# Kernel optimization log

Hardware: AMD Instinct MI355X
Metric: run time of the kernel (lower is better)

The kernel has to match this reference:

```python
import jax, jax.numpy as jnp
import numpy as np

S = 72
IMG_W, IMG_H = 640, 360
STRIDE = 32
FMAP_H, FMAP_W = IMG_H // STRIDE, IMG_W // STRIDE  # 11, 20
N_OFFSETS = S
N_STRIPS = S - 1
ANGLES = np.array([15.0, 22.0, 30.0, 39.0, 49.0, 60.0, 72.0, 80.0, 90.0, 100.0, 108.0, 120.0, 131.0, 141.0, 150.0, 158.0, 165.0])
N_ANG = 17
N_PRED = 2 + 2 + 1 + N_OFFSETS  # 77
N_EDGE = FMAP_W + 2 * FMAP_H    # 42
N_PROP = N_ANG * N_EDGE         # 714
NMS_THRES = 15.0
BACKBONE_C = 512
CONV_C = 1024


def _make_anchors():
    anchor_ys = np.linspace(1.0, 0.0, N_OFFSETS)
    tan = np.tan(np.deg2rad(ANGLES))
    def side(origins):
        out = np.zeros((N_ANG, N_PRED, len(origins)), np.float32)
        for i, (sx, sy) in enumerate(origins):
            out[:, 2, i] = 1.0 - sy
            out[:, 3, i] = sx
            out[:, 5:, i] = (sx + (sy - anchor_ys)[None, :] / tan[:, None]) * IMG_W
        return out.reshape(N_ANG * N_PRED, len(origins))
    left = side([(0.0, y) for y in np.linspace(1.0, 0.0, FMAP_H)])
    right = side([(1.0, y) for y in np.linspace(1.0, 0.0, FMAP_H)])
    bottom = side([(x, 1.0) for x in np.linspace(1.0, 0.0, FMAP_W)])
    anchors = np.zeros((N_ANG * N_PRED, FMAP_H, FMAP_W), np.float32)
    anchors[:, :, 0] = left
    anchors[:, :, -1] = right
    anchors[:, -1, :] = bottom
    edge = np.concatenate([anchors[:, :, 0], anchors[:, :, -1], anchors[:, -1, :]], 1)  # [1309,42]
    anch_dim = edge.reshape(N_ANG, N_PRED, N_EDGE).transpose(2, 0, 1).reshape(N_PROP, N_PRED)
    return jnp.asarray(anchors), jnp.asarray(anch_dim)


def setup_inputs():
    key = jax.random.key(0)
    ks = jax.random.split(key, 4)
    B = 32
    feat = jax.random.normal(ks[0], (B, BACKBONE_C, FMAP_H, FMAP_W), jnp.float32)
    W_conv = jax.random.normal(ks[1], (CONV_C, BACKBONE_C), jnp.float32) * 0.02
    b_conv = jnp.zeros((CONV_C,), jnp.float32)
    W_cls = jax.random.normal(ks[2], (2 * N_ANG, CONV_C), jnp.float32) * 0.02
    b_cls = jnp.zeros((2 * N_ANG,), jnp.float32)
    W_reg = jax.random.normal(ks[3], (N_ANG * (N_OFFSETS + 1), CONV_C), jnp.float32) * 0.02
    b_reg = jnp.zeros((N_ANG * (N_OFFSETS + 1),), jnp.float32)
    anchors, anchors_anchor_dim = _make_anchors()
    return {"feat": feat, "W_conv": W_conv, "b_conv": b_conv, "W_cls": W_cls, "b_cls": b_cls,
            "W_reg": W_reg, "b_reg": b_reg, "anchors": anchors, "anchors_anchor_dim": anchors_anchor_dim}


def _proposals(feat, W_conv, b_conv, W_cls, b_cls, W_reg, b_reg, anchors):
    B = feat.shape[0]
    features = jnp.einsum('bchw,oc->bohw', feat, W_conv) + b_conv[None, :, None, None]
    cls_f = jnp.einsum('bchw,oc->bohw', features, W_cls) + b_cls[None, :, None, None]
    reg_f = jnp.einsum('bchw,oc->bohw', features, W_reg) + b_reg[None, :, None, None]
    anch = anchors.reshape(N_ANG, N_PRED, FMAP_H, FMAP_W)
    cls_r = cls_f.reshape(B, N_ANG, 2, FMAP_H, FMAP_W)
    reg_r = reg_f.reshape(B, N_ANG, N_OFFSETS + 1, FMAP_H, FMAP_W)
    # slots 0:2 <- cls logits (set), slots 2:4 <- anchor (copied), slots 4: <- anchor + reg
    mid = jnp.broadcast_to(anch[None, :, 2:4], (B, N_ANG, 2, FMAP_H, FMAP_W))
    tail = anch[None, :, 4:] + reg_r
    lane = jnp.concatenate([cls_r, mid, tail], axis=2)  # [B,17,77,h,w]
    # gather the three feature-map edges: left col, right col, bottom row
    edges = jnp.concatenate([lane[:, :, :, :, 0], lane[:, :, :, :, -1], lane[:, :, :, -1, :]], axis=3)  # [B,17,77,42]
    return edges.transpose(0, 3, 1, 2).reshape(B, N_PROP, N_PRED)  # [B,714,77]


def _nms_one(props, scores):
    # greedy line-NMS over proposals of one image, shapes static
    order = jnp.argsort(-scores)
    p = props[order]
    start = jnp.clip(jnp.round(p[:, 2] * N_STRIPS), 0.0, float(N_STRIPS))
    end = jnp.clip(start + p[:, 4] - 1.0, 0.0, float(N_STRIPS))
    xs = p[:, 5:]  # [N,72]
    s = jnp.maximum(start[:, None], start[None, :])
    e = jnp.minimum(end[:, None], end[None, :])
    idx = jnp.arange(N_OFFSETS, dtype=p.dtype)
    m = (idx[None, None, :] >= s[..., None]) & (idx[None, None, :] <= e[..., None])  # [N,N,72]
    diff = jnp.abs(xs[:, None, :] - xs[None, :, :])  # [N,N,72]
    cnt = e - s + 1.0
    dist = jnp.where(cnt > 0, jnp.sum(diff * m, -1) / jnp.maximum(cnt, 1.0), jnp.inf)
    sup = dist < NMS_THRES
    n = p.shape[0]
    pos = jnp.arange(n)
    def step(suppressed, i):
        keep_i = ~suppressed[i]
        suppressed = suppressed | (keep_i & sup[i] & (pos > i))
        return suppressed, keep_i
    _, keep_sorted = jax.lax.scan(step, jnp.zeros(n, bool), pos)
    return jnp.zeros(n, bool).at[order].set(keep_sorted)


def reference(feat, W_conv, b_conv, W_cls, b_cls, W_reg, b_reg, anchors, anchors_anchor_dim):
    proposals = _proposals(feat, W_conv, b_conv, W_cls, b_cls, W_reg, b_reg, anchors)
    scores = jax.nn.softmax(proposals[..., :2], axis=-1)[..., 1]  # [B,714]
    keep_mask = jax.lax.map(lambda pr: _nms_one(pr[0], pr[1]), (proposals, scores))  # [B,714]
    return proposals, keep_mask, scores
```

## Files before the change

kernel.cpp:

```cpp
#include <hip/hip_runtime.h>
#include <math.h>

#define NB     32
#define FH     11
#define FW     20
#define CIN    512
#define CMID   1024
#define NANG   17
#define NPREDD 77
#define NEDGE  42
#define NPROPP 714
#define NOFF   72
#define NCLS   34
#define NREGR  1241
#define N2PAD  1280
#define MTOT   1344
#define NSTRIPSF 71.0f
#define PADK   40

typedef unsigned long long u64;
typedef unsigned short ushortt;
typedef short s8v __attribute__((ext_vector_type(8)));
typedef float f4v __attribute__((ext_vector_type(4)));

__device__ inline ushortt f2bf(float f) {
    unsigned u = __float_as_uint(f);
    u += 0x7fffu + ((u >> 16) & 1u);
    return (ushortt)(u >> 16);
}
__device__ inline float bf2f(ushortt h) {
    return __uint_as_float(((unsigned)h) << 16);
}

__global__ __launch_bounds__(256) void k_gather_split(const float* __restrict__ feat,
                                                      ushortt* __restrict__ Ahi,
                                                      ushortt* __restrict__ Alo)
{
    int idx = blockIdx.x * 256 + threadIdx.x;
    int m = idx >> 9, c = idx & 511;
    int b = m / NEDGE, e = m - b * NEDGE;
    int h, w;
    if (e < FH)          { h = e;      w = 0;      }
    else if (e < 2 * FH) { h = e - FH; w = FW - 1; }
    else                 { h = FH - 1; w = e - 2 * FH; }
    float v = feat[((size_t)(b * CIN + c) * FH + h) * FW + w];
    ushortt hi = f2bf(v);
    Ahi[idx] = hi;
    Alo[idx] = f2bf(v - bf2f(hi));
}

__global__ __launch_bounds__(256) void k_gemm1m(const ushortt* __restrict__ Ahi,
                                                const ushortt* __restrict__ Alo,
                                                const float* __restrict__ W,
                                                const float* __restrict__ bias,
                                                ushortt* __restrict__ Chi,
                                                ushortt* __restrict__ Clo)
{
    const int K = CIN, N = CMID;
    __shared__ __align__(16) ushortt Ash[64 * PADK], Asl[64 * PADK];
    __shared__ __align__(16) ushortt Bsh[64 * PADK], Bsl[64 * PADK];
    int tid = threadIdx.x;
    int m0 = blockIdx.y * 64, n0 = blockIdx.x * 64;
    int srow = tid >> 2, sg = tid & 3;
    int lane = tid & 63, wv = tid >> 6;
    int wm = (wv & 1) * 32, wn = (wv >> 1) * 32;
    int quad = lane >> 4, l15 = lane & 15;

    f4v acc[2][2];
#pragma unroll
    for (int i = 0; i < 2; ++i)
#pragma unroll
        for (int j = 0; j < 2; ++j) acc[i][j] = (f4v){0.f, 0.f, 0.f, 0.f};

    const ushortt* Ahp = Ahi + (size_t)(m0 + srow) * K + sg * 8;
    const ushortt* Alp = Alo + (size_t)(m0 + srow) * K + sg * 8;
    const float*   Wp  = W   + (size_t)(n0 + srow) * K + sg * 8;

    for (int k0 = 0; k0 < K; k0 += 32) {
        __syncthreads();
        s8v av = *(const s8v*)(Ahp + k0);
        s8v lv = *(const s8v*)(Alp + k0);
        float4 w0 = *(const float4*)(Wp + k0);
        float4 w1 = *(const float4*)(Wp + k0 + 4);
        float wf[8] = {w0.x, w0.y, w0.z, w0.w, w1.x, w1.y, w1.z, w1.w};
        s8v wh, wl;
#pragma unroll
        for (int j = 0; j < 8; ++j) {
            ushortt h = f2bf(wf[j]);
            wh[j] = (short)h;
            wl[j] = (short)f2bf(wf[j] - bf2f(h));
        }
        *(s8v*)&Ash[srow * PADK + sg * 8] = av;
        *(s8v*)&Asl[srow * PADK + sg * 8] = lv;
        *(s8v*)&Bsh[srow * PADK + sg * 8] = wh;
        *(s8v*)&Bsl[srow * PADK + sg * 8] = wl;
        __syncthreads();
        s8v ah[2], al[2], bh[2], bl[2];
#pragma unroll
        for (int s = 0; s < 2; ++s) {
            ah[s] = *(const s8v*)&Ash[(wm + s * 16 + l15) * PADK + quad * 8];
            al[s] = *(const s8v*)&Asl[(wm + s * 16 + l15) * PADK + quad * 8];
            bh[s] = *(const s8v*)&Bsh[(wn + s * 16 + l15) * PADK + quad * 8];
            bl[s] = *(const s8v*)&Bsl[(wn + s * 16 + l15) * PADK + quad * 8];
        }
#pragma unroll
        for (int sm = 0; sm < 2; ++sm)
#pragma unroll
            for (int sn = 0; sn < 2; ++sn) {
                acc[sm][sn] = __builtin_amdgcn_mfma_f32_16x16x32_bf16(al[sm], bl[sn], acc[sm][sn], 0, 0, 0);
                acc[sm][sn] = __builtin_amdgcn_mfma_f32_16x16x32_bf16(al[sm], bh[sn], acc[sm][sn], 0, 0, 0);
                acc[sm][sn] = __builtin_amdgcn_mfma_f32_16x16x32_bf16(ah[sm], bl[sn], acc[sm][sn], 0, 0, 0);
                acc[sm][sn] = __builtin_amdgcn_mfma_f32_16x16x32_bf16(ah[sm], bh[sn], acc[sm][sn], 0, 0, 0);
            }
    }
#pragma unroll
    for (int sm = 0; sm < 2; ++sm)
#pragma unroll
        for (int sn = 0; sn < 2; ++sn)
#pragma unroll
            for (int r = 0; r < 4; ++r) {
                int m = m0 + wm + sm * 16 + quad * 4 + r;
                int n = n0 + wn + sn * 16 + l15;
                float v = acc[sm][sn][r] + bias[n];
                ushortt h = f2bf(v);
                Chi[(size_t)m * N + n] = h;
                Clo[(size_t)m * N + n] = f2bf(v - bf2f(h));
            }
}

__global__ __launch_bounds__(256) void k_gemm2m(const ushortt* __restrict__ Ahi,
                                                const ushortt* __restrict__ Alo,
                                                const float* __restrict__ Wcls,
                                                const float* __restrict__ bcls,
                                                const float* __restrict__ Wreg,
                                                const float* __restrict__ breg,
                                                float* __restrict__ C)
{
    const int K = CMID;
    __shared__ __align__(16) ushortt Ash[64 * PADK], Asl[64 * PADK];
    __shared__ __align__(16) ushortt Bsh[64 * PADK], Bsl[64 * PADK];
    int tid = threadIdx.x;
    int m0 = blockIdx.y * 64, n0 = blockIdx.x * 64;
    int srow = tid >> 2, sg = tid & 3;
    int lane = tid & 63, wv = tid >> 6;
    int wm = (wv & 1) * 32, wn = (wv >> 1) * 32;
    int quad = lane >> 4, l15 = lane & 15;

    f4v acc[2][2];
#pragma unroll
    for (int i = 0; i < 2; ++i)
#pragma unroll
        for (int j = 0; j < 2; ++j) acc[i][j] = (f4v){0.f, 0.f, 0.f, 0.f};

    const ushortt* Ahp = Ahi + (size_t)(m0 + srow) * K + sg * 8;
    const ushortt* Alp = Alo + (size_t)(m0 + srow) * K + sg * 8;
    int nrow = n0 + srow;
    const float* Wp = Wcls;
    bool wvalid = true;
    if (nrow < NCLS)              Wp = Wcls + (size_t)nrow * K + sg * 8;
    else if (nrow < NCLS + NREGR) Wp = Wreg + (size_t)(nrow - NCLS) * K + sg * 8;
    else                          wvalid = false;

    for (int k0 = 0; k0 < K; k0 += 32) {
        __syncthreads();
        s8v av = *(const s8v*)(Ahp + k0);
        s8v lv = *(const s8v*)(Alp + k0);
        float4 w0, w1;
        if (wvalid) {
            w0 = *(const float4*)(Wp + k0);
            w1 = *(const float4*)(Wp + k0 + 4);
        } else {
            w0 = make_float4(0.f, 0.f, 0.f, 0.f);
            w1 = w0;
        }
        float wf[8] = {w0.x, w0.y, w0.z, w0.w, w1.x, w1.y, w1.z, w1.w};
        s8v wh, wl;
#pragma unroll
        for (int j = 0; j < 8; ++j) {
            ushortt h = f2bf(wf[j]);
            wh[j] = (short)h;
            wl[j] = (short)f2bf(wf[j] - bf2f(h));
        }
        *(s8v*)&Ash[srow * PADK + sg * 8] = av;
        *(s8v*)&Asl[srow * PADK + sg * 8] = lv;
        *(s8v*)&Bsh[srow * PADK + sg * 8] = wh;
        *(s8v*)&Bsl[srow * PADK + sg * 8] = wl;
        __syncthreads();
        s8v ah[2], al[2], bh[2], bl[2];
#pragma unroll
        for (int s = 0; s < 2; ++s) {
            ah[s] = *(const s8v*)&Ash[(wm + s * 16 + l15) * PADK + quad * 8];
            al[s] = *(const s8v*)&Asl[(wm + s * 16 + l15) * PADK + quad * 8];
            bh[s] = *(const s8v*)&Bsh[(wn + s * 16 + l15) * PADK + quad * 8];
            bl[s] = *(const s8v*)&Bsl[(wn + s * 16 + l15) * PADK + quad * 8];
        }
#pragma unroll
        for (int sm = 0; sm < 2; ++sm)
#pragma unroll
            for (int sn = 0; sn < 2; ++sn) {
                acc[sm][sn] = __builtin_amdgcn_mfma_f32_16x16x32_bf16(al[sm], bl[sn], acc[sm][sn], 0, 0, 0);
                acc[sm][sn] = __builtin_amdgcn_mfma_f32_16x16x32_bf16(al[sm], bh[sn], acc[sm][sn], 0, 0, 0);
                acc[sm][sn] = __builtin_amdgcn_mfma_f32_16x16x32_bf16(ah[sm], bl[sn], acc[sm][sn], 0, 0, 0);
                acc[sm][sn] = __builtin_amdgcn_mfma_f32_16x16x32_bf16(ah[sm], bh[sn], acc[sm][sn], 0, 0, 0);
            }
    }
#pragma unroll
    for (int sm = 0; sm < 2; ++sm)
#pragma unroll
        for (int sn = 0; sn < 2; ++sn)
#pragma unroll
            for (int r = 0; r < 4; ++r) {
                int m = m0 + wm + sm * 16 + quad * 4 + r;
                int n = n0 + wn + sn * 16 + l15;
                float bb = (n < NCLS) ? bcls[n] : ((n < NCLS + NREGR) ? breg[n - NCLS] : 0.f);
                C[(size_t)m * N2PAD + n] = acc[sm][sn][r] + bb;
            }
}

__global__ __launch_bounds__(256) void k_assemble(const float* __restrict__ C2,
                                                  const float* __restrict__ AD,
                                                  float* __restrict__ outP,
                                                  float* __restrict__ outS,
                                                  float* __restrict__ startv,
                                                  float* __restrict__ endv,
                                                  float* __restrict__ xsel)
{
    int mb = blockIdx.x;
    int b = mb / NEDGE, e = mb - b * NEDGE;
    const float* c2 = C2 + (size_t)mb * N2PAD;
    int tid = threadIdx.x;
    for (int idx = tid; idx < NANG * NPREDD; idx += 256) {
        int a = idx / NPREDD, p = idx - a * NPREDD;
        int prop = e * NANG + a;
        float v;
        if (p < 2) v = c2[a * 2 + p];
        else {
            v = AD[prop * NPREDD + p];
            if (p >= 4) v += c2[NCLS + a * 73 + (p - 4)];
        }
        outP[((size_t)b * NPROPP + prop) * NPREDD + p] = v;
    }
    if (tid < NANG) {
        int a = tid, prop = e * NANG + a;
        float c0 = c2[2 * a], c1 = c2[2 * a + 1];
        float mx = fmaxf(c0, c1);
        float e0 = expf(c0 - mx), e1 = expf(c1 - mx);
        outS[b * NPROPP + prop] = e1 / (e0 + e1);
        float p2 = AD[prop * NPREDD + 2];
        float p4 = AD[prop * NPREDD + 4] + c2[NCLS + a * 73];
        float st = fminf(fmaxf(rintf(p2 * NSTRIPSF), 0.0f), NSTRIPSF);
        float en = fminf(fmaxf(st + p4 - 1.0f, 0.0f), NSTRIPSF);
        startv[b * 720 + prop] = st;
        endv[b * 720 + prop] = en;
        int ksi = (int)st;
        xsel[b * 720 + prop] = AD[prop * NPREDD + 5 + ksi] + c2[NCLS + a * 73 + ksi + 1];
    }
}

__global__ __launch_bounds__(128) void k_sort(const float* __restrict__ scores,
                                              int* __restrict__ order)
{
    int b = blockIdx.x, tile = blockIdx.y, tid = threadIdx.x;
    __shared__ __align__(16) float s[720];
    for (int x = tid; x < 720; x += 128)
        s[x] = (x < NPROPP) ? scores[b * NPROPP + x] : -1e30f;
    __syncthreads();
    int i = tile * 128 + tid;
    if (i >= NPROPP) return;
    float si = s[i];
    int r = 0;
#pragma unroll 4
    for (int j4 = 0; j4 < 720; j4 += 4) {
        float4 v = *(const float4*)&s[j4];
        r += (v.x > si) || (v.x == si && (j4 + 0) < i);
        r += (v.y > si) || (v.y == si && (j4 + 1) < i);
        r += (v.z > si) || (v.z == si && (j4 + 2) < i);
        r += (v.w > si) || (v.w == si && (j4 + 3) < i);
    }
    order[b * 720 + r] = i;
}

__global__ __launch_bounds__(256) void k_supmat(const float* __restrict__ outP,
                                                const float* __restrict__ startv,
                                                const float* __restrict__ endv,
                                                const float* __restrict__ xsel,
                                                const int* __restrict__ order,
                                                u64* __restrict__ sup)
{
    int jt = blockIdx.x, it = blockIdx.y, b = blockIdx.z;
    int i0 = it * 64, j0 = jt * 64;
    int tid = threadIdx.x;
    if (j0 + 63 < i0) {
        if (tid < 64) {
            int il = i0 + tid;
            if (il < NPROPP) sup[((size_t)b * NPROPP + il) * 12 + jt] = 0ull;
        }
        return;
    }
    __shared__ float SI[64], EI[64], XI[64];
    __shared__ float SJ[64], EJ[64], XJ[64];
    __shared__ int   OI[64], OJ[64];
    if (tid < 128) {
        int side = tid >> 6, q = tid & 63;
        int pos = (side ? j0 : i0) + q;
        int o = (pos < NPROPP) ? order[b * 720 + pos] : -1;
        float st = (o >= 0) ? startv[b * 720 + o] : 0.f;
        float en = (o >= 0) ? endv[b * 720 + o] : -2.f;
        float xv = (o >= 0) ? xsel[b * 720 + o] : 0.f;
        if (!side) { SI[q] = st; EI[q] = en; XI[q] = xv; OI[q] = o; }
        else       { SJ[q] = st; EJ[q] = en; XJ[q] = xv; OJ[q] = o; }
    }
    __syncthreads();
    int lane = tid & 63, w = tid >> 6;
    int j = j0 + lane;
    float sj = SJ[lane], ej = EJ[lane], xj = XJ[lane];
    const float* basexs = outP + (size_t)b * NPROPP * NPREDD + 5;
#pragma unroll 1
    for (int rep = 0; rep < 16; ++rep) {
        int iloc = w * 16 + rep;
        int il = i0 + iloc;
        float si = SI[iloc], ei = EI[iloc];
        float s = fmaxf(si, sj), e = fminf(ei, ej);
        float cnt = e - s + 1.0f;
        bool sp = false;
        if (cnt > 0.f) {
            if (e < s) {
                sp = true;
            } else {
                int ks = (int)s, ke = (int)e;
                if (si == sj && ke == ks) {
                    sp = (fabsf(XI[iloc] - xj) / fmaxf(cnt, 1.0f)) < 15.0f;
                } else {
                    const float* xi  = basexs + (size_t)OI[iloc] * NPREDD;
                    const float* xjp = basexs + (size_t)OJ[lane] * NPREDD;
                    float sum = 0.f;
                    for (int k = ks; k <= ke; ++k)
                        sum += fabsf(xi[k] - xjp[k]);
                    sp = (sum / fmaxf(cnt, 1.0f)) < 15.0f;
                }
            }
        }
        bool valid = (il < NPROPP) && (j < NPROPP) && (j > il);
        u64 msk = __ballot(valid && sp);
        if (lane == 0 && il < NPROPP)
            sup[((size_t)b * NPROPP + il) * 12 + jt] = msk;
    }
}

__global__ __launch_bounds__(256) void k_scan(const u64* __restrict__ sup,
                                              const int* __restrict__ order,
                                              float* __restrict__ keep_out)
{
    int b = blockIdx.x, tid = threadIdx.x;
    int lane = tid & 63;
    __shared__ u64 K[12], NS[12];
    __shared__ int changed;
    const u64* base = sup + (size_t)b * NPROPP * 12;

    int r0 = tid, r1 = tid + 256, r2 = tid + 512;
    u64 row0[12], row1[12], row2[12];
#pragma unroll
    for (int t = 0; t < 12; ++t) {
        row0[t] = base[(size_t)r0 * 12 + t];
        row1[t] = (r1 < NPROPP) ? base[(size_t)r1 * 12 + t] : 0ull;
        row2[t] = (r2 < NPROPP) ? base[(size_t)r2 * 12 + t] : 0ull;
    }
    if (tid < 12) {
        K[tid] = (tid < 11) ? ~0ull : ((1ull << (NPROPP - 704)) - 1ull);
        NS[tid] = 0ull;
    }
    __syncthreads();

    for (int sweep = 0; sweep < 720; ++sweep) {
        u64 m0 = 0ull - ((K[r0 >> 6] >> (r0 & 63)) & 1ull);
        u64 m1 = (r1 < NPROPP) ? (0ull - ((K[r1 >> 6] >> (r1 & 63)) & 1ull)) : 0ull;
        u64 m2 = (r2 < NPROPP) ? (0ull - ((K[r2 >> 6] >> (r2 & 63)) & 1ull)) : 0ull;
        unsigned lo[12], hi[12];
#pragma unroll
        for (int t = 0; t < 12; ++t) {
            u64 a = (row0[t] & m0) | (row1[t] & m1) | (row2[t] & m2);
            lo[t] = (unsigned)a;
            hi[t] = (unsigned)(a >> 32);
        }
#pragma unroll
        for (int s = 1; s < 64; s <<= 1) {
#pragma unroll
            for (int t = 0; t < 12; ++t) {
                lo[t] |= __shfl_xor(lo[t], s, 64);
                hi[t] |= __shfl_xor(hi[t], s, 64);
            }
        }
        if (tid == 0) changed = 0;
        if (lane == 0) {
#pragma unroll
            for (int t = 0; t < 12; ++t)
                atomicOr(&NS[t], ((u64)hi[t] << 32) | (u64)lo[t]);
        }
        __syncthreads();
        if (tid < 12) {
            u64 valid = (tid < 11) ? ~0ull : ((1ull << (NPROPP - 704)) - 1ull);
            u64 nk = valid & ~NS[tid];
            if (nk != K[tid]) changed = 1;
            K[tid] = nk;
            NS[tid] = 0ull;
        }
        __syncthreads();
        if (!changed) break;
    }
    if (r0 < NPROPP)
        keep_out[b * NPROPP + order[b * 720 + r0]] =
            ((K[r0 >> 6] >> (r0 & 63)) & 1ull) ? 1.f : 0.f;
    if (r1 < NPROPP)
        keep_out[b * NPROPP + order[b * 720 + r1]] =
            ((K[r1 >> 6] >> (r1 & 63)) & 1ull) ? 1.f : 0.f;
    if (r2 < NPROPP)
        keep_out[b * NPROPP + order[b * 720 + r2]] =
            ((K[r2 >> 6] >> (r2 & 63)) & 1ull) ? 1.f : 0.f;
}

extern "C" void kernel_launch(void* const* d_in, const int* in_sizes, int n_in,
                              void* d_out, int out_size, void* d_ws, size_t ws_size,
                              hipStream_t stream)
{
    const float* feat  = (const float*)d_in[0];
    const float* Wconv = (const float*)d_in[1];
    const float* bconv = (const float*)d_in[2];
    const float* Wcls  = (const float*)d_in[3];
    const float* bcls  = (const float*)d_in[4];
    const float* Wreg  = (const float*)d_in[5];
    const float* breg  = (const float*)d_in[6];
    const float* AD    = (const float*)d_in[8];

    float* out  = (float*)d_out;
    float* outP = out;
    float* outK = out + (size_t)NB * NPROPP * NPREDD;
    float* outS = outK + (size_t)NB * NPROPP;

    float* ws = (float*)d_ws;
    ushortt* A1hi = (ushortt*)ws;
    ushortt* A1lo = (ushortt*)(ws + 344064);
    ushortt* A2hi = (ushortt*)(ws + 688128);
    ushortt* A2lo = (ushortt*)(ws + 1376256);
    float*   C2   = ws + 2064384;
    float* startv = ws;
    float* endv   = ws + 23040;
    int*   order  = (int*)(ws + 46080);
    u64*   sup    = (u64*)(ws + 69120);
    float* xsel   = ws + 617472;

    k_gather_split<<<dim3(2688),       dim3(256), 0, stream>>>(feat, A1hi, A1lo);
    k_gemm1m      <<<dim3(16, 21),     dim3(256), 0, stream>>>(A1hi, A1lo, Wconv, bconv, A2hi, A2lo);
    k_gemm2m      <<<dim3(20, 21),     dim3(256), 0, stream>>>(A2hi, A2lo, Wcls, bcls, Wreg, breg, C2);
    k_assemble    <<<dim3(MTOT),       dim3(256), 0, stream>>>(C2, AD, outP, outS, startv, endv, xsel);
    k_sort        <<<dim3(NB, 6),      dim3(128), 0, stream>>>(outS, order);
    k_supmat      <<<dim3(12, 12, NB), dim3(256), 0, stream>>>(outP, startv, endv, xsel, order, sup);
    k_scan        <<<dim3(NB),         dim3(256), 0, stream>>>(sup, order, outK);
}
```

Before: 192.8 us.

## Pre-split weights to bf16 hi/lo once and double-buffer GEMM shared tiles

Weight matrices are now converted to bf16 hi/lo pairs in a single prep kernel that also does the feature gather, instead of each GEMM tile converting fp32 weights every k-step. Both GEMMs now use double-buffered shared memory with register prefetch of the next k-slice, so there is one barrier per iteration instead of two. This removes repeated conversion work, since each weight element was split once per M-tile. It adds extra global traffic to write and reread the split weights, and doubles shared memory per block.

```diff
diff --git a/kernel.cpp b/kernel.cpp
--- a/kernel.cpp
+++ b/kernel.cpp
@@ -21,6 +21,7 @@
 typedef unsigned long long u64;
 typedef unsigned short ushortt;
 typedef short s8v __attribute__((ext_vector_type(8)));
+typedef ushortt u4v __attribute__((ext_vector_type(4)));
 typedef float f4v __attribute__((ext_vector_type(4)));
 
 __device__ inline ushortt f2bf(float f) {
@@ -32,39 +33,80 @@
     return __uint_as_float(((unsigned)h) << 16);
 }
 
-__global__ __launch_bounds__(256) void k_gather_split(const float* __restrict__ feat,
-                                                      ushortt* __restrict__ Ahi,
-                                                      ushortt* __restrict__ Alo)
-{
-    int idx = blockIdx.x * 256 + threadIdx.x;
-    int m = idx >> 9, c = idx & 511;
-    int b = m / NEDGE, e = m - b * NEDGE;
-    int h, w;
-    if (e < FH)          { h = e;      w = 0;      }
-    else if (e < 2 * FH) { h = e - FH; w = FW - 1; }
-    else                 { h = FH - 1; w = e - 2 * FH; }
-    float v = feat[((size_t)(b * CIN + c) * FH + h) * FW + w];
-    ushortt hi = f2bf(v);
-    Ahi[idx] = hi;
-    Alo[idx] = f2bf(v - bf2f(hi));
+__global__ __launch_bounds__(256) void k_prep(const float* __restrict__ feat,
+                                              ushortt* __restrict__ A1hi,
+                                              ushortt* __restrict__ A1lo,
+                                              const float* __restrict__ Wconv,
+                                              ushortt* __restrict__ B1h,
+                                              ushortt* __restrict__ B1l,
+                                              const float* __restrict__ Wcls,
+                                              const float* __restrict__ Wreg,
+                                              ushortt* __restrict__ B2h,
+                                              ushortt* __restrict__ B2l)
+{
+    int bid = blockIdx.x, tid = threadIdx.x;
+    if (bid < 2688) {
+        int idx = bid * 256 + tid;
+        int m = idx >> 9, c = idx & 511;
+        int b = m / NEDGE, e = m - b * NEDGE;
+        int h, w;
+        if (e < FH)          { h = e;      w = 0;      }
+        else if (e < 2 * FH) { h = e - FH; w = FW - 1; }
+        else                 { h = FH - 1; w = e - 2 * FH; }
+        float v = feat[((size_t)(b * CIN + c) * FH + h) * FW + w];
+        ushortt hi = f2bf(v);
+        A1hi[idx] = hi;
+        A1lo[idx] = f2bf(v - bf2f(hi));
+    } else if (bid < 2688 + 512) {
+        int t = (bid - 2688) * 256 + tid;
+        float4 v = *(const float4*)(Wconv + (size_t)t * 4);
+        float vf[4] = {v.x, v.y, v.z, v.w};
+        u4v hv, lv;
+#pragma unroll
+        for (int j = 0; j < 4; ++j) {
+            ushortt h = f2bf(vf[j]);
+            hv[j] = h;
+            lv[j] = f2bf(vf[j] - bf2f(h));
+        }
+        *(u4v*)(B1h + (size_t)t * 4) = hv;
+        *(u4v*)(B1l + (size_t)t * 4) = lv;
+    } else {
+        int t = (bid - 3200) * 256 + tid;
+        int row = t >> 8, col = (t & 255) * 4;
+        float4 v = make_float4(0.f, 0.f, 0.f, 0.f);
+        if (row < NCLS)              v = *(const float4*)(Wcls + (size_t)row * CMID + col);
+        else if (row < NCLS + NREGR) v = *(const float4*)(Wreg + (size_t)(row - NCLS) * CMID + col);
+        float vf[4] = {v.x, v.y, v.z, v.w};
+        u4v hv, lv;
+#pragma unroll
+        for (int j = 0; j < 4; ++j) {
+            ushortt h = f2bf(vf[j]);
+            hv[j] = h;
+            lv[j] = f2bf(vf[j] - bf2f(h));
+        }
+        *(u4v*)(B2h + (size_t)t * 4) = hv;
+        *(u4v*)(B2l + (size_t)t * 4) = lv;
+    }
 }
 
 __global__ __launch_bounds__(256) void k_gemm1m(const ushortt* __restrict__ Ahi,
                                                 const ushortt* __restrict__ Alo,
-                                                const float* __restrict__ W,
+                                                const ushortt* __restrict__ Bh,
+                                                const ushortt* __restrict__ Bl,
                                                 const float* __restrict__ bias,
                                                 ushortt* __restrict__ Chi,
                                                 ushortt* __restrict__ Clo)
 {
     const int K = CIN, N = CMID;
-    __shared__ __align__(16) ushortt Ash[64 * PADK], Asl[64 * PADK];
-    __shared__ __align__(16) ushortt Bsh[64 * PADK], Bsl[64 * PADK];
+    __shared__ __align__(16) ushortt Ash[2][64 * PADK], Asl[2][64 * PADK];
+    __shared__ __align__(16) ushortt Bsh[2][64 * PADK], Bsl[2][64 * PADK];
     int tid = threadIdx.x;
     int m0 = blockIdx.y * 64, n0 = blockIdx.x * 64;
     int srow = tid >> 2, sg = tid & 3;
     int lane = tid & 63, wv = tid >> 6;
     int wm = (wv & 1) * 32, wn = (wv >> 1) * 32;
     int quad = lane >> 4, l15 = lane & 15;
+    int wo = srow * PADK + sg * 8;
 
     f4v acc[2][2];
 #pragma unroll
@@ -74,34 +116,35 @@
 
     const ushortt* Ahp = Ahi + (size_t)(m0 + srow) * K + sg * 8;
     const ushortt* Alp = Alo + (size_t)(m0 + srow) * K + sg * 8;
-    const float*   Wp  = W   + (size_t)(n0 + srow) * K + sg * 8;
-
+    const ushortt* Bhp = Bh  + (size_t)(n0 + srow) * K + sg * 8;
+    const ushortt* Blp = Bl  + (size_t)(n0 + srow) * K + sg * 8;
+
+    s8v ra = *(const s8v*)Ahp;
+    s8v rl = *(const s8v*)Alp;
+    s8v rb = *(const s8v*)Bhp;
+    s8v rc = *(const s8v*)Blp;
+    *(s8v*)&Ash[0][wo] = ra;
+    *(s8v*)&Asl[0][wo] = rl;
+    *(s8v*)&Bsh[0][wo] = rb;
+    *(s8v*)&Bsl[0][wo] = rc;
+    __syncthreads();
+
+    int buf = 0;
     for (int k0 = 0; k0 < K; k0 += 32) {
-        __syncthreads();
-        s8v av = *(const s8v*)(Ahp + k0);
-        s8v lv = *(const s8v*)(Alp + k0);
-        float4 w0 = *(const float4*)(Wp + k0);
-        float4 w1 = *(const float4*)(Wp + k0 + 4);
-        float wf[8] = {w0.x, w0.y, w0.z, w0.w, w1.x, w1.y, w1.z, w1.w};
-        s8v wh, wl;
-#pragma unroll
-        for (int j = 0; j < 8; ++j) {
-            ushortt h = f2bf(wf[j]);
-            wh[j] = (short)h;
-            wl[j] = (short)f2bf(wf[j] - bf2f(h));
-        }
-        *(s8v*)&Ash[srow * PADK + sg * 8] = av;
-        *(s8v*)&Asl[srow * PADK + sg * 8] = lv;
-        *(s8v*)&Bsh[srow * PADK + sg * 8] = wh;
-        *(s8v*)&Bsl[srow * PADK + sg * 8] = wl;
-        __syncthreads();
+        bool more = (k0 + 32 < K);
+        if (more) {
+            ra = *(const s8v*)(Ahp + k0 + 32);
+            rl = *(const s8v*)(Alp + k0 + 32);
+            rb = *(const s8v*)(Bhp + k0 + 32);
+            rc = *(const s8v*)(Blp + k0 + 32);
+        }
         s8v ah[2], al[2], bh[2], bl[2];
 #pragma unroll
         for (int s = 0; s < 2; ++s) {
-            ah[s] = *(const s8v*)&Ash[(wm + s * 16 + l15) * PADK + quad * 8];
-            al[s] = *(const s8v*)&Asl[(wm + s * 16 + l15) * PADK + quad * 8];
-            bh[s] = *(const s8v*)&Bsh[(wn + s * 16 + l15) * PADK + quad * 8];
-            bl[s] = *(const s8v*)&Bsl[(wn + s * 16 + l15) * PADK + quad * 8];
+            ah[s] = *(const s8v*)&Ash[buf][(wm + s * 16 + l15) * PADK + quad * 8];
+            al[s] = *(const s8v*)&Asl[buf][(wm + s * 16 + l15) * PADK + quad * 8];
+            bh[s] = *(const s8v*)&Bsh[buf][(wn + s * 16 + l15) * PADK + quad * 8];
+            bl[s] = *(const s8v*)&Bsl[buf][(wn + s * 16 + l15) * PADK + quad * 8];
         }
 #pragma unroll
         for (int sm = 0; sm < 2; ++sm)
@@ -112,6 +155,14 @@
                 acc[sm][sn] = __builtin_amdgcn_mfma_f32_16x16x32_bf16(ah[sm], bl[sn], acc[sm][sn], 0, 0, 0);
                 acc[sm][sn] = __builtin_amdgcn_mfma_f32_16x16x32_bf16(ah[sm], bh[sn], acc[sm][sn], 0, 0, 0);
             }
+        if (more) {
+            *(s8v*)&Ash[buf ^ 1][wo] = ra;
+            *(s8v*)&Asl[buf ^ 1][wo] = rl;
+            *(s8v*)&Bsh[buf ^ 1][wo] = rb;
+            *(s8v*)&Bsl[buf ^ 1][wo] = rc;
+        }
+        __syncthreads();
+        buf ^= 1;
     }
 #pragma unroll
     for (int sm = 0; sm < 2; ++sm)
@@ -130,21 +181,22 @@
 
 __global__ __launch_bounds__(256) void k_gemm2m(const ushortt* __restrict__ Ahi,
                                                 const ushortt* __restrict__ Alo,
-                                                const float* __restrict__ Wcls,
+                                                const ushortt* __restrict__ Bh,
+                                                const ushortt* __restrict__ Bl,
                                                 const float* __restrict__ bcls,
-                                                const float* __restrict__ Wreg,
                                                 const float* __restrict__ breg,
                                                 float* __restrict__ C)
 {
     const int K = CMID;
-    __shared__ __align__(16) ushortt Ash[64 * PADK], Asl[64 * PADK];
-    __shared__ __align__(16) ushortt Bsh[64 * PADK], Bsl[64 * PADK];
+    __shared__ __align__(16) ushortt Ash[2][64 * PADK], Asl[2][64 * PADK];
+    __shared__ __align__(16) ushortt Bsh[2][64 * PADK], Bsl[2][64 * PADK];
     int tid = threadIdx.x;
     int m0 = blockIdx.y * 64, n0 = blockIdx.x * 64;
     int srow = tid >> 2, sg = tid & 3;
     int lane = tid & 63, wv = tid >> 6;
     int wm = (wv & 1) * 32, wn = (wv >> 1) * 32;
     int quad = lane >> 4, l15 = lane & 15;
+    int wo = srow * PADK + sg * 8;
 
     f4v acc[2][2];
 #pragma unroll
@@ -154,45 +206,35 @@
 
     const ushortt* Ahp = Ahi + (size_t)(m0 + srow) * K + sg * 8;
     const ushortt* Alp = Alo + (size_t)(m0 + srow) * K + sg * 8;
-    int nrow = n0 + srow;
-    const float* Wp = Wcls;
-    bool wvalid = true;
-    if (nrow < NCLS)              Wp = Wcls + (size_t)nrow * K + sg * 8;
-    else if (nrow < NCLS + NREGR) Wp = Wreg + (size_t)(nrow - NCLS) * K + sg * 8;
-    else                          wvalid = false;
-
+    const ushortt* Bhp = Bh  + (size_t)(n0 + srow) * K + sg * 8;
+    const ushortt* Blp = Bl  + (size_t)(n0 + srow) * K + sg * 8;
+
+    s8v ra = *(const s8v*)Ahp;
+    s8v rl = *(const s8v*)Alp;
+    s8v rb = *(const s8v*)Bhp;
+    s8v rc = *(const s8v*)Blp;
+    *(s8v*)&Ash[0][wo] = ra;
+    *(s8v*)&Asl[0][wo] = rl;
+    *(s8v*)&Bsh[0][wo] = rb;
+    *(s8v*)&Bsl[0][wo] = rc;
+    __syncthreads();
+
+    int buf = 0;
     for (int k0 = 0; k0 < K; k0 += 32) {
-        __syncthreads();
-        s8v av = *(const s8v*)(Ahp + k0);
-        s8v lv = *(const s8v*)(Alp + k0);
-        float4 w0, w1;
-        if (wvalid) {
-            w0 = *(const float4*)(Wp + k0);
-            w1 = *(const float4*)(Wp + k0 + 4);
-        } else {
-            w0 = make_float4(0.f, 0.f, 0.f, 0.f);
-            w1 = w0;
-        }
-        float wf[8] = {w0.x, w0.y, w0.z, w0.w, w1.x, w1.y, w1.z, w1.w};
-        s8v wh, wl;
-#pragma unroll
-        for (int j = 0; j < 8; ++j) {
-            ushortt h = f2bf(wf[j]);
-            wh[j] = (short)h;
-            wl[j] = (short)f2bf(wf[j] - bf2f(h));
-        }
-        *(s8v*)&Ash[srow * PADK + sg * 8] = av;
-        *(s8v*)&Asl[srow * PADK + sg * 8] = lv;
-        *(s8v*)&Bsh[srow * PADK + sg * 8] = wh;
-        *(s8v*)&Bsl[srow * PADK + sg * 8] = wl;
-        __syncthreads();
+        bool more = (k0 + 32 < K);
+        if (more) {
+            ra = *(const s8v*)(Ahp + k0 + 32);
+            rl = *(const s8v*)(Alp + k0 + 32);
+            rb = *(const s8v*)(Bhp + k0 + 32);
+            rc = *(const s8v*)(Blp + k0 + 32);
+        }
         s8v ah[2], al[2], bh[2], bl[2];
 #pragma unroll
         for (int s = 0; s < 2; ++s) {
-            ah[s] = *(const s8v*)&Ash[(wm + s * 16 + l15) * PADK + quad * 8];
-            al[s] = *(const s8v*)&Asl[(wm + s * 16 + l15) * PADK + quad * 8];
-            bh[s] = *(const s8v*)&Bsh[(wn + s * 16 + l15) * PADK + quad * 8];
-            bl[s] = *(const s8v*)&Bsl[(wn + s * 16 + l15) * PADK + quad * 8];
+            ah[s] = *(const s8v*)&Ash[buf][(wm + s * 16 + l15) * PADK + quad * 8];
+            al[s] = *(const s8v*)&Asl[buf][(wm + s * 16 + l15) * PADK + quad * 8];
+            bh[s] = *(const s8v*)&Bsh[buf][(wn + s * 16 + l15) * PADK + quad * 8];
+            bl[s] = *(const s8v*)&Bsl[buf][(wn + s * 16 + l15) * PADK + quad * 8];
         }
 #pragma unroll
         for (int sm = 0; sm < 2; ++sm)
@@ -203,6 +245,14 @@
                 acc[sm][sn] = __builtin_amdgcn_mfma_f32_16x16x32_bf16(ah[sm], bl[sn], acc[sm][sn], 0, 0, 0);
                 acc[sm][sn] = __builtin_amdgcn_mfma_f32_16x16x32_bf16(ah[sm], bh[sn], acc[sm][sn], 0, 0, 0);
             }
+        if (more) {
+            *(s8v*)&Ash[buf ^ 1][wo] = ra;
+            *(s8v*)&Asl[buf ^ 1][wo] = rl;
+            *(s8v*)&Bsh[buf ^ 1][wo] = rb;
+            *(s8v*)&Bsl[buf ^ 1][wo] = rc;
+        }
+        __syncthreads();
+        buf ^= 1;
     }
 #pragma unroll
     for (int sm = 0; sm < 2; ++sm)
@@ -442,15 +492,21 @@
     ushortt* A2hi = (ushortt*)(ws + 688128);
     ushortt* A2lo = (ushortt*)(ws + 1376256);
     float*   C2   = ws + 2064384;
+    ushortt* B1h  = (ushortt*)(ws + 3784704);
+    ushortt* B1l  = (ushortt*)(ws + 4046848);
+    ushortt* B2h  = (ushortt*)(ws + 4308992);
+    ushortt* B2l  = (ushortt*)(ws + 4964352);
     float* startv = ws;
     float* endv   = ws + 23040;
     int*   order  = (int*)(ws + 46080);
     u64*   sup    = (u64*)(ws + 69120);
     float* xsel   = ws + 617472;
 
-    k_gather_split<<<dim3(2688),       dim3(256), 0, stream>>>(feat, A1hi, A1lo);
-    k_gemm1m      <<<dim3(16, 21),     dim3(256), 0, stream>>>(A1hi, A1lo, Wconv, bconv, A2hi, A2lo);
-    k_gemm2m      <<<dim3(20, 21),     dim3(256), 0, stream>>>(A2hi, A2lo, Wcls, bcls, Wreg, breg, C2);
+    k_prep        <<<dim3(4480),       dim3(256), 0, stream>>>(feat, A1hi, A1lo,
+                                                               Wconv, B1h, B1l,
+                                                               Wcls, Wreg, B2h, B2l);
+    k_gemm1m      <<<dim3(16, 21),     dim3(256), 0, stream>>>(A1hi, A1lo, B1h, B1l, bconv, A2hi, A2lo);
+    k_gemm2m      <<<dim3(20, 21),     dim3(256), 0, stream>>>(A2hi, A2lo, B2h, B2l, bcls, breg, C2);
     k_assemble    <<<dim3(MTOT),       dim3(256), 0, stream>>>(C2, AD, outP, outS, startv, endv, xsel);
     k_sort        <<<dim3(NB, 6),      dim3(128), 0, stream>>>(outS, order);
     k_supmat      <<<dim3(12, 12, NB), dim3(256), 0, stream>>>(outP, startv, endv, xsel, order, sup);
```

Result: faster. 185.0 us (-4.0%).
